# Performance work log

Hardware: AMD Instinct MI355X
Metric: run time of the kernel (lower is better)

## Reference

```python
import jax, jax.numpy as jnp
import numpy as np

N_NODES = 65536
N_EDGES = 1048576
D_IN = 1024
D_HID = 64
N_CLS = 32


def gcn_conv(x, W, b, src, dst, n_nodes):
    """PyG GCNConv: linear transform, then symmetric-normalized aggregation
    with implicit self-loops (fill value 1)."""
    xw = x @ W  # [N, d_out]
    e = src.shape[0]
    # degree over destination index, including the self-loop (+1)
    deg = jax.ops.segment_sum(jnp.ones((e,), xw.dtype), dst, num_segments=n_nodes) + 1.0
    dinv_sqrt = jax.lax.rsqrt(deg)  # deg >= 1, safe
    norm = dinv_sqrt[src] * dinv_sqrt[dst]  # [E]
    agg = jax.ops.segment_sum(xw[src] * norm[:, None], dst, num_segments=n_nodes)
    # self-loop contribution: norm = deg_i^{-1}
    agg = agg + xw * (1.0 / deg)[:, None]
    return agg + b


def setup_inputs() -> dict:
    key = jax.random.key(0)
    k_x, k_e, k_w1, k_b1, k_w2, k_b2 = jax.random.split(key, 6)
    x = jax.random.normal(k_x, (N_NODES, D_IN), dtype=jnp.float32)
    edge_index = jax.random.randint(k_e, (2, N_EDGES), 0, N_NODES, dtype=jnp.int64)
    s1 = 1.0 / np.sqrt(D_IN)
    s2 = 1.0 / np.sqrt(D_HID)
    W1 = jax.random.uniform(k_w1, (D_IN, D_HID), jnp.float32, -s1, s1)
    b1 = jax.random.uniform(k_b1, (D_HID,), jnp.float32, -s1, s1)
    W2 = jax.random.uniform(k_w2, (D_HID, N_CLS), jnp.float32, -s2, s2)
    b2 = jax.random.uniform(k_b2, (N_CLS,), jnp.float32, -s2, s2)
    return {"x": x, "edge_index": edge_index, "W1": W1, "b1": b1, "W2": W2, "b2": b2}


def reference(x, edge_index, W1, b1, W2, b2):
    src, dst = edge_index[0], edge_index[1]
    n = x.shape[0]
    h = gcn_conv(x, W1, b1, src, dst, n)
    h = jax.nn.relu(h)
    # dropout is identity in eval mode
    h = gcn_conv(h, W2, b2, src, dst, n)
    return jax.nn.log_softmax(h, axis=1)
```

## Files before the change

kernel.cpp:

```cpp
#include <hip/hip_runtime.h>
#include <hip/hip_bf16.h>

#define N_NODES 65536
#define D_IN 1024
#define D_HID 64
#define N_CLS 32

typedef short short8 __attribute__((ext_vector_type(8)));
typedef float floatx4 __attribute__((ext_vector_type(4)));

__device__ __forceinline__ unsigned short f2bf(float f) {
  union { float f; unsigned u; } cv; cv.f = f;
  unsigned r = (cv.u + 0x7FFFu + ((cv.u >> 16) & 1u)) >> 16;
  return (unsigned short)r;
}
__device__ __forceinline__ float2 bf2f2(unsigned v) {
  union { unsigned u; float f; } a, b;
  a.u = v << 16;
  b.u = v & 0xFFFF0000u;
  return make_float2(a.f, b.f);
}

__global__ void k_count_w1t(const int* __restrict__ dst, int* __restrict__ cnt,
                            const float* __restrict__ w1, unsigned short* __restrict__ w1t,
                            int e4) {
  int b = blockIdx.x;
  if (b >= 1024) {
    int i = (b - 1024) * 256 + threadIdx.x;
    int k = i / D_HID, n = i % D_HID;
    w1t[n * D_IN + k] = f2bf(w1[i]);
    return;
  }
  int i = b * 256 + threadIdx.x;
  if (i < e4) {
    int4 d = ((const int4*)dst)[i];
    atomicAdd(&cnt[d.x], 1);
    atomicAdd(&cnt[d.y], 1);
    atomicAdd(&cnt[d.z], 1);
    atomicAdd(&cnt[d.w], 1);
  }
}

__global__ void k_scan_a(const int* __restrict__ cnt, int* __restrict__ bsum) {
  __shared__ int s[256];
  int t = threadIdx.x;
  s[t] = cnt[blockIdx.x * 256 + t];
  __syncthreads();
  for (int off = 128; off > 0; off >>= 1) {
    if (t < off) s[t] += s[t + off];
    __syncthreads();
  }
  if (t == 0) bsum[blockIdx.x] = s[0];
}

__global__ void k_scan_c(const int* __restrict__ cnt, const int* __restrict__ bsum,
                         int* __restrict__ rowptr, int* __restrict__ cursor,
                         float* __restrict__ dinv) {
  __shared__ int s[256];
  int t = threadIdx.x;
  s[t] = (t < blockIdx.x) ? bsum[t] : 0;
  __syncthreads();
  for (int off = 128; off > 0; off >>= 1) {
    if (t < off) s[t] += s[t + off];
    __syncthreads();
  }
  int blockoff = s[0];
  __syncthreads();
  int i = blockIdx.x * 256 + t;
  int v = cnt[i];
  s[t] = v;
  __syncthreads();
  for (int off = 1; off < 256; off <<= 1) {
    int x = (t >= off) ? s[t - off] : 0;
    __syncthreads();
    s[t] += x;
    __syncthreads();
  }
  int excl = s[t] - v + blockoff;
  rowptr[i] = excl;
  cursor[i] = excl;
  dinv[i] = rsqrtf((float)(v + 1));
  if (i == N_NODES - 1) rowptr[N_NODES] = excl + v;
}

__global__ __launch_bounds__(256) void k_fill_gemm1(
    const int* __restrict__ src, const int* __restrict__ dst,
    int* __restrict__ cursor, int* __restrict__ csr_src, int e4,
    const float* __restrict__ x, const unsigned short* __restrict__ w1t,
    const float* __restrict__ dinv, unsigned short* __restrict__ xw1s) {
  if (blockIdx.x >= 1024) {
    int i = (blockIdx.x - 1024) * 256 + threadIdx.x;
    int e8 = e4 >> 1;
    if (i < e8) {
      const int4* d4 = (const int4*)dst;
      const int4* s4 = (const int4*)src;
      int4 da = d4[2 * i], db = d4[2 * i + 1];
      int4 sa = s4[2 * i], sb = s4[2 * i + 1];
      int p0 = atomicAdd(&cursor[da.x], 1);
      int p1 = atomicAdd(&cursor[da.y], 1);
      int p2 = atomicAdd(&cursor[da.z], 1);
      int p3 = atomicAdd(&cursor[da.w], 1);
      int p4 = atomicAdd(&cursor[db.x], 1);
      int p5 = atomicAdd(&cursor[db.y], 1);
      int p6 = atomicAdd(&cursor[db.z], 1);
      int p7 = atomicAdd(&cursor[db.w], 1);
      csr_src[p0] = sa.x; csr_src[p1] = sa.y;
      csr_src[p2] = sa.z; csr_src[p3] = sa.w;
      csr_src[p4] = sb.x; csr_src[p5] = sb.y;
      csr_src[p6] = sb.z; csr_src[p7] = sb.w;
    }
    return;
  }
  int wave = threadIdx.x >> 6;
  int lane = threadIdx.x & 63;
  int quad = lane >> 4;
  int l16 = lane & 15;
  int rowbase = blockIdx.x * 64 + wave * 16;
  const float* xrow = x + (size_t)(rowbase + l16) * D_IN + quad * 8;
  const unsigned short* bbase = w1t + quad * 8;
  floatx4 acc[4];
#pragma unroll
  for (int nt = 0; nt < 4; nt++) acc[nt] = (floatx4){0.f, 0.f, 0.f, 0.f};
  float4 p0 = *(const float4*)(xrow + 0);
  float4 p1 = *(const float4*)(xrow + 4);
  float4 p2 = *(const float4*)(xrow + 32);
  float4 p3 = *(const float4*)(xrow + 36);
  for (int k0 = 0; k0 < D_IN; k0 += 64) {
    float4 c0 = p0, c1 = p1, c2 = p2, c3 = p3;
    if (k0 + 64 < D_IN) {
      p0 = *(const float4*)(xrow + k0 + 64);
      p1 = *(const float4*)(xrow + k0 + 68);
      p2 = *(const float4*)(xrow + k0 + 96);
      p3 = *(const float4*)(xrow + k0 + 100);
    }
    float av0[8] = {c0.x, c0.y, c0.z, c0.w, c1.x, c1.y, c1.z, c1.w};
    float av1[8] = {c2.x, c2.y, c2.z, c2.w, c3.x, c3.y, c3.z, c3.w};
    short8 af0, af1;
    unsigned* u0 = (unsigned*)&af0;
    unsigned* u1 = (unsigned*)&af1;
#pragma unroll
    for (int j = 0; j < 4; j++) {
      asm("v_cvt_pk_bf16_f32 %0, %1, %2" : "=v"(u0[j]) : "v"(av0[2 * j]), "v"(av0[2 * j + 1]));
      asm("v_cvt_pk_bf16_f32 %0, %1, %2" : "=v"(u1[j]) : "v"(av1[2 * j]), "v"(av1[2 * j + 1]));
    }
    short8 bf0[4], bf1[4];
#pragma unroll
    for (int nt = 0; nt < 4; nt++) {
      const unsigned short* bp = bbase + (size_t)(nt * 16 + l16) * D_IN + k0;
      bf0[nt] = *(const short8*)(bp);
      bf1[nt] = *(const short8*)(bp + 32);
    }
#pragma unroll
    for (int nt = 0; nt < 4; nt++)
      acc[nt] = __builtin_amdgcn_mfma_f32_16x16x32_bf16(af0, bf0[nt], acc[nt], 0, 0, 0);
#pragma unroll
    for (int nt = 0; nt < 4; nt++)
      acc[nt] = __builtin_amdgcn_mfma_f32_16x16x32_bf16(af1, bf1[nt], acc[nt], 0, 0, 0);
  }
#pragma unroll
  for (int r = 0; r < 4; r++) {
    int row = rowbase + quad * 4 + r;
    float sc = dinv[row];
#pragma unroll
    for (int nt = 0; nt < 4; nt++)
      xw1s[(size_t)row * D_HID + nt * 16 + l16] = f2bf(acc[nt][r] * sc);
  }
}

__global__ __launch_bounds__(256) void k_agg1(const unsigned* __restrict__ xw1s2,
    const int* __restrict__ rowptr, const int* __restrict__ csr_src,
    const float* __restrict__ dinv, const float* __restrict__ b1,
    const float* __restrict__ w2, unsigned short* __restrict__ xw2s) {
  __shared__ float w2s[D_HID * N_CLS];
  for (int i = threadIdx.x; i < D_HID * N_CLS; i += 256) w2s[i] = w2[i];
  __syncthreads();
  int wave = threadIdx.x >> 6;
  int lane = threadIdx.x & 63;
  int h = lane >> 5, l = lane & 31;
  int node = blockIdx.x * 4 + wave;
  float dd = dinv[node];
  int beg = rowptr[node], end = rowptr[node + 1];
  float cx[8], cy[8];
#pragma unroll
  for (int j = 0; j < 8; j++) { cx[j] = 0.f; cy[j] = 0.f; }
  for (int e = beg + h; e < end; e += 16) {
    int idx[8]; bool val[8];
#pragma unroll
    for (int j = 0; j < 8; j++) {
      int ee = e + 2 * j;
      val[j] = ee < end;
      idx[j] = csr_src[val[j] ? ee : beg];
    }
#pragma unroll
    for (int j = 0; j < 8; j++) {
      float2 v = bf2f2(xw1s2[(size_t)idx[j] * 32 + l]);
      cx[j] += val[j] ? v.x : 0.f;
      cy[j] += val[j] ? v.y : 0.f;
    }
  }
  float sx = ((cx[0] + cx[1]) + (cx[2] + cx[3])) + ((cx[4] + cx[5]) + (cx[6] + cx[7]));
  float sy = ((cy[0] + cy[1]) + (cy[2] + cy[3])) + ((cy[4] + cy[5]) + (cy[6] + cy[7]));
  sx += __shfl_xor(sx, 32);
  sy += __shfl_xor(sy, 32);
  float2 self = bf2f2(xw1s2[(size_t)node * 32 + l]);
  float2 bb = ((const float2*)b1)[l];
  float vx = dd * (sx + self.x) + bb.x;
  float vy = dd * (sy + self.y) + bb.y;
  vx = vx > 0.f ? vx : 0.f;
  vy = vy > 0.f ? vy : 0.f;
  int c = lane & 31;
  float p = 0.f;
#pragma unroll
  for (int kk = 0; kk < 32; kk++) {
    int k = h * 32 + kk;
    float hv = (k & 1) ? __shfl(vy, k >> 1) : __shfl(vx, k >> 1);
    p += hv * w2s[k * N_CLS + c];
  }
  p += __shfl_xor(p, 32);
  if (lane < 32) xw2s[(size_t)node * N_CLS + c] = f2bf(p * dd);
}

__global__ __launch_bounds__(256) void k_agg2(const unsigned* __restrict__ xw2s2,
    const int* __restrict__ rowptr, const int* __restrict__ csr_src,
    const float* __restrict__ dinv, const float* __restrict__ b2,
    float* __restrict__ out) {
  int wave = threadIdx.x >> 6;
  int lane = threadIdx.x & 63;
  int q = lane >> 4, l = lane & 15;
  int node = blockIdx.x * 4 + wave;
  float dd = dinv[node];
  int beg = rowptr[node], end = rowptr[node + 1];
  float cx[4], cy[4];
#pragma unroll
  for (int j = 0; j < 4; j++) { cx[j] = 0.f; cy[j] = 0.f; }
  for (int e = beg + q; e < end; e += 16) {
    int idx[4]; bool val[4];
#pragma unroll
    for (int j = 0; j < 4; j++) {
      int ee = e + 4 * j;
      val[j] = ee < end;
      idx[j] = csr_src[val[j] ? ee : beg];
    }
#pragma unroll
    for (int j = 0; j < 4; j++) {
      float2 v = bf2f2(xw2s2[(size_t)idx[j] * 16 + l]);
      cx[j] += val[j] ? v.x : 0.f;
      cy[j] += val[j] ? v.y : 0.f;
    }
  }
  float sx = (cx[0] + cx[1]) + (cx[2] + cx[3]);
  float sy = (cy[0] + cy[1]) + (cy[2] + cy[3]);
  sx += __shfl_xor(sx, 32); sy += __shfl_xor(sy, 32);
  sx += __shfl_xor(sx, 16); sy += __shfl_xor(sy, 16);
  float2 self = bf2f2(xw2s2[(size_t)node * 16 + l]);
  float2 bb = ((const float2*)b2)[l];
  float lx = dd * (sx + self.x) + bb.x;
  float ly = dd * (sy + self.y) + bb.y;
  float m = fmaxf(lx, ly);
#pragma unroll
  for (int o = 8; o > 0; o >>= 1) m = fmaxf(m, __shfl_xor(m, o));
  float s2 = __expf(lx - m) + __expf(ly - m);
#pragma unroll
  for (int o = 8; o > 0; o >>= 1) s2 += __shfl_xor(s2, o);
  float lse = m + __logf(s2);
  if (lane < 16)
    ((float2*)out)[(size_t)node * 16 + l] = make_float2(lx - lse, ly - lse);
}

extern "C" void kernel_launch(void* const* d_in, const int* in_sizes, int n_in,
                              void* d_out, int out_size, void* d_ws, size_t ws_size,
                              hipStream_t stream) {
  (void)n_in; (void)out_size; (void)ws_size;
  const float* x  = (const float*)d_in[0];
  const int*   ei = (const int*)d_in[1];
  const float* w1 = (const float*)d_in[2];
  const float* b1 = (const float*)d_in[3];
  const float* w2 = (const float*)d_in[4];
  const float* b2 = (const float*)d_in[5];
  float* out = (float*)d_out;
  int e = in_sizes[1] / 2;
  const int* src = ei;
  const int* dst = ei + e;

  char* ws = (char*)d_ws;
  int* cnt            = (int*)(ws + 0x000000);
  int* rowptr         = (int*)(ws + 0x040000);
  int* cursor         = (int*)(ws + 0x0C0000);
  float* dinv         = (float*)(ws + 0x100000);
  int* bsum           = (int*)(ws + 0x140000);
  int* csr_src        = (int*)(ws + 0x180000);
  unsigned short* w1t = (unsigned short*)(ws + 0x580000);
  unsigned short* xw1s= (unsigned short*)(ws + 0x600000);
  unsigned short* xw2s= (unsigned short*)(ws + 0xE00000);

  int e4 = e / 4;
  hipMemsetAsync(cnt, 0, N_NODES * sizeof(int), stream);
  k_count_w1t<<<1280, 256, 0, stream>>>(dst, cnt, w1, w1t, e4);
  k_scan_a   <<<N_NODES / 256, 256, 0, stream>>>(cnt, bsum);
  k_scan_c   <<<N_NODES / 256, 256, 0, stream>>>(cnt, bsum, rowptr, cursor, dinv);
  k_fill_gemm1<<<1536, 256, 0, stream>>>(src, dst, cursor, csr_src, e4,
                                         x, w1t, dinv, xw1s);
  k_agg1     <<<N_NODES / 4, 256, 0, stream>>>((const unsigned*)xw1s, rowptr, csr_src,
                                               dinv, b1, w2, xw2s);
  k_agg2     <<<N_NODES / 4, 256, 0, stream>>>((const unsigned*)xw2s, rowptr, csr_src,
                                               dinv, b2, out);
}
```

Baseline: 553.0 us.

## Pad atomic counters to separate cache lines and software-pipeline W1 loads in GEMM

```diff
diff --git a/kernel.cpp b/kernel.cpp
--- a/kernel.cpp
+++ b/kernel.cpp
@@ -5,6 +5,7 @@
 #define D_IN 1024
 #define D_HID 64
 #define N_CLS 32
+#define CPAD 5
 
 typedef short short8 __attribute__((ext_vector_type(8)));
 typedef float floatx4 __attribute__((ext_vector_type(4)));
@@ -34,17 +35,17 @@
   int i = b * 256 + threadIdx.x;
   if (i < e4) {
     int4 d = ((const int4*)dst)[i];
-    atomicAdd(&cnt[d.x], 1);
-    atomicAdd(&cnt[d.y], 1);
-    atomicAdd(&cnt[d.z], 1);
-    atomicAdd(&cnt[d.w], 1);
+    atomicAdd(&cnt[d.x << CPAD], 1);
+    atomicAdd(&cnt[d.y << CPAD], 1);
+    atomicAdd(&cnt[d.z << CPAD], 1);
+    atomicAdd(&cnt[d.w << CPAD], 1);
   }
 }
 
 __global__ void k_scan_a(const int* __restrict__ cnt, int* __restrict__ bsum) {
   __shared__ int s[256];
   int t = threadIdx.x;
-  s[t] = cnt[blockIdx.x * 256 + t];
+  s[t] = cnt[(blockIdx.x * 256 + t) << CPAD];
   __syncthreads();
   for (int off = 128; off > 0; off >>= 1) {
     if (t < off) s[t] += s[t + off];
@@ -67,7 +68,7 @@
   int blockoff = s[0];
   __syncthreads();
   int i = blockIdx.x * 256 + t;
-  int v = cnt[i];
+  int v = cnt[i << CPAD];
   s[t] = v;
   __syncthreads();
   for (int off = 1; off < 256; off <<= 1) {
@@ -78,7 +79,7 @@
   }
   int excl = s[t] - v + blockoff;
   rowptr[i] = excl;
-  cursor[i] = excl;
+  cursor[i << CPAD] = excl;
   dinv[i] = rsqrtf((float)(v + 1));
   if (i == N_NODES - 1) rowptr[N_NODES] = excl + v;
 }
@@ -96,14 +97,14 @@
       const int4* s4 = (const int4*)src;
       int4 da = d4[2 * i], db = d4[2 * i + 1];
       int4 sa = s4[2 * i], sb = s4[2 * i + 1];
-      int p0 = atomicAdd(&cursor[da.x], 1);
-      int p1 = atomicAdd(&cursor[da.y], 1);
-      int p2 = atomicAdd(&cursor[da.z], 1);
-      int p3 = atomicAdd(&cursor[da.w], 1);
-      int p4 = atomicAdd(&cursor[db.x], 1);
-      int p5 = atomicAdd(&cursor[db.y], 1);
-      int p6 = atomicAdd(&cursor[db.z], 1);
-      int p7 = atomicAdd(&cursor[db.w], 1);
+      int p0 = atomicAdd(&cursor[da.x << CPAD], 1);
+      int p1 = atomicAdd(&cursor[da.y << CPAD], 1);
+      int p2 = atomicAdd(&cursor[da.z << CPAD], 1);
+      int p3 = atomicAdd(&cursor[da.w << CPAD], 1);
+      int p4 = atomicAdd(&cursor[db.x << CPAD], 1);
+      int p5 = atomicAdd(&cursor[db.y << CPAD], 1);
+      int p6 = atomicAdd(&cursor[db.z << CPAD], 1);
+      int p7 = atomicAdd(&cursor[db.w << CPAD], 1);
       csr_src[p0] = sa.x; csr_src[p1] = sa.y;
       csr_src[p2] = sa.z; csr_src[p3] = sa.w;
       csr_src[p4] = sb.x; csr_src[p5] = sb.y;
@@ -125,14 +126,20 @@
   float4 p1 = *(const float4*)(xrow + 4);
   float4 p2 = *(const float4*)(xrow + 32);
   float4 p3 = *(const float4*)(xrow + 36);
+  short8 bf0[4], bf1[4];
+#pragma unroll
+  for (int nt = 0; nt < 4; nt++) {
+    const unsigned short* bp = bbase + (size_t)(nt * 16 + l16) * D_IN;
+    bf0[nt] = *(const short8*)(bp);
+    bf1[nt] = *(const short8*)(bp + 32);
+  }
   for (int k0 = 0; k0 < D_IN; k0 += 64) {
     float4 c0 = p0, c1 = p1, c2 = p2, c3 = p3;
-    if (k0 + 64 < D_IN) {
-      p0 = *(const float4*)(xrow + k0 + 64);
-      p1 = *(const float4*)(xrow + k0 + 68);
-      p2 = *(const float4*)(xrow + k0 + 96);
-      p3 = *(const float4*)(xrow + k0 + 100);
-    }
+    int kn = (k0 + 64 < D_IN) ? k0 + 64 : k0;
+    p0 = *(const float4*)(xrow + kn);
+    p1 = *(const float4*)(xrow + kn + 4);
+    p2 = *(const float4*)(xrow + kn + 32);
+    p3 = *(const float4*)(xrow + kn + 36);
     float av0[8] = {c0.x, c0.y, c0.z, c0.w, c1.x, c1.y, c1.z, c1.w};
     float av1[8] = {c2.x, c2.y, c2.z, c2.w, c3.x, c3.y, c3.z, c3.w};
     short8 af0, af1;
@@ -143,19 +150,18 @@
       asm("v_cvt_pk_bf16_f32 %0, %1, %2" : "=v"(u0[j]) : "v"(av0[2 * j]), "v"(av0[2 * j + 1]));
       asm("v_cvt_pk_bf16_f32 %0, %1, %2" : "=v"(u1[j]) : "v"(av1[2 * j]), "v"(av1[2 * j + 1]));
     }
-    short8 bf0[4], bf1[4];
-#pragma unroll
-    for (int nt = 0; nt < 4; nt++) {
-      const unsigned short* bp = bbase + (size_t)(nt * 16 + l16) * D_IN + k0;
-      bf0[nt] = *(const short8*)(bp);
-      bf1[nt] = *(const short8*)(bp + 32);
-    }
 #pragma unroll
     for (int nt = 0; nt < 4; nt++)
       acc[nt] = __builtin_amdgcn_mfma_f32_16x16x32_bf16(af0, bf0[nt], acc[nt], 0, 0, 0);
 #pragma unroll
     for (int nt = 0; nt < 4; nt++)
+      bf0[nt] = *(const short8*)(bbase + (size_t)(nt * 16 + l16) * D_IN + kn);
+#pragma unroll
+    for (int nt = 0; nt < 4; nt++)
       acc[nt] = __builtin_amdgcn_mfma_f32_16x16x32_bf16(af1, bf1[nt], acc[nt], 0, 0, 0);
+#pragma unroll
+    for (int nt = 0; nt < 4; nt++)
+      bf1[nt] = *(const short8*)(bbase + (size_t)(nt * 16 + l16) * D_IN + kn + 32);
   }
 #pragma unroll
   for (int r = 0; r < 4; r++) {
@@ -283,18 +289,18 @@
   const int* dst = ei + e;
 
   char* ws = (char*)d_ws;
-  int* cnt            = (int*)(ws + 0x000000);
-  int* rowptr         = (int*)(ws + 0x040000);
-  int* cursor         = (int*)(ws + 0x0C0000);
-  float* dinv         = (float*)(ws + 0x100000);
-  int* bsum           = (int*)(ws + 0x140000);
-  int* csr_src        = (int*)(ws + 0x180000);
-  unsigned short* w1t = (unsigned short*)(ws + 0x580000);
-  unsigned short* xw1s= (unsigned short*)(ws + 0x600000);
-  unsigned short* xw2s= (unsigned short*)(ws + 0xE00000);
+  int* cnt            = (int*)(ws + 0x0000000);
+  int* cursor         = (int*)(ws + 0x0800000);
+  int* rowptr         = (int*)(ws + 0x1000000);
+  float* dinv         = (float*)(ws + 0x1050000);
+  int* bsum           = (int*)(ws + 0x1090000);
+  int* csr_src        = (int*)(ws + 0x10A0000);
+  unsigned short* w1t = (unsigned short*)(ws + 0x14A0000);
+  unsigned short* xw1s= (unsigned short*)(ws + 0x14C0000);
+  unsigned short* xw2s= (unsigned short*)(ws + 0x1CC0000);
 
   int e4 = e / 4;
-  hipMemsetAsync(cnt, 0, N_NODES * sizeof(int), stream);
+  hipMemsetAsync(cnt, 0, (size_t)N_NODES * 32 * sizeof(int), stream);
   k_count_w1t<<<1280, 256, 0, stream>>>(dst, cnt, w1, w1t, e4);
   k_scan_a   <<<N_NODES / 256, 256, 0, stream>>>(cnt, bsum);
   k_scan_c   <<<N_NODES / 256, 256, 0, stream>>>(cnt, bsum, rowptr, cursor, dinv);
```

After: 549.1 us. No clear change (-0.7%).
